# Kernel optimization log

Hardware: AMD Instinct MI355X
Metric: run time of the kernel (lower is better)

The kernel has to match this reference:

```python
import jax, jax.numpy as jnp
import numpy as np
import math

N_HEADS = 8

def setup_inputs() -> dict:
    key = jax.random.key(0)
    ks = jax.random.split(key, 5)
    B, S, D = 2, 2048, 512
    return {
        "x": jax.random.normal(ks[0], (B, S, D), dtype=jnp.float32),
        "w_in": jax.random.normal(ks[1], (3 * D, D), dtype=jnp.float32) * (1.0 / math.sqrt(D)),
        "b_in": jax.random.normal(ks[2], (3 * D,), dtype=jnp.float32) * 0.01,
        "w_out": jax.random.normal(ks[3], (D, D), dtype=jnp.float32) * (1.0 / math.sqrt(D)),
        "b_out": jax.random.normal(ks[4], (D,), dtype=jnp.float32) * 0.01,
        "casual_mask": 1,
    }

def reference(x, w_in, b_in, w_out, b_out, casual_mask):
    B, S, D = x.shape
    H = N_HEADS
    dh = D // H
    # in_proj: torch Linear -> x @ W.T + b
    qvk = x @ w_in.T + b_in  # [B, S, 3D]
    # NOTE: source unpacks as q, v, k (chunk order quirk preserved)
    q, v, k = jnp.split(qvk, 3, axis=-1)
    # [B, S, D] -> [B, H, S, dh]
    def to_heads(t):
        return t.reshape(B, S, H, dh).transpose(0, 2, 1, 3)
    q, k, v = to_heads(q), to_heads(k), to_heads(v)
    scores = jnp.einsum("bhqd,bhkd->bhqk", q, k)  # [B, H, S, S]
    if casual_mask:
        # mask BEFORE scaling, as in the source (-inf unaffected by division)
        tri = jnp.triu(jnp.ones((S, S), dtype=bool), k=1)
        scores = jnp.where(tri, -jnp.inf, scores)
    scores = scores / math.sqrt(dh)
    attn = jax.nn.softmax(scores, axis=-1)
    out = jnp.einsum("bhqk,bhkd->bhqd", attn, v)  # [B, H, S, dh]
    out = out.transpose(0, 2, 1, 3).reshape(B, S, D)
    return out @ w_out.T + b_out
```

## Files before the change

### kernel.cpp

```cpp
#include <hip/hip_runtime.h>
#include <hip/hip_bf16.h>

typedef unsigned short u16;
typedef unsigned int u32;
typedef __attribute__((ext_vector_type(8))) short bf16x8;
typedef __attribute__((ext_vector_type(4))) short bf16x4;
typedef __attribute__((ext_vector_type(4))) float f32x4;

#define DEVI __device__ __forceinline__

DEVI u16 f2bf(float f) {
  union { float f; unsigned int u; } v; v.f = f;
  unsigned int u = v.u;
  unsigned int r = (u + 0x7fffu + ((u >> 16) & 1u)) >> 16;
  return (u16)r;
}

DEVI float fexp2(float x) {
#if __has_builtin(__builtin_amdgcn_exp2f)
  return __builtin_amdgcn_exp2f(x);
#else
  return exp2f(x);
#endif
}

DEVI void lds_cp16(u16* lds, const u16* g) {
  __builtin_amdgcn_global_load_lds(
      (const __attribute__((address_space(1))) u32*)g,
      (__attribute__((address_space(3))) u32*)lds, 16, 0, 0);
}

DEVI f32x4 mfma16x16x16_bf16(bf16x4 a, bf16x4 b, f32x4 c) {
#if __has_builtin(__builtin_amdgcn_mfma_f32_16x16x16bf16_1k)
  return __builtin_amdgcn_mfma_f32_16x16x16bf16_1k(a, b, c, 0, 0, 0);
#else
  f32x4 d;
  asm volatile("v_mfma_f32_16x16x16_bf16 %0, %1, %2, %3"
               : "=v"(d) : "v"(a), "v"(b), "v"(c));
  return d;
#endif
}

__global__ __launch_bounds__(256) void cvt_all(
    const float4* __restrict__ x, const float4* __restrict__ wi,
    const float4* __restrict__ wo, u16* __restrict__ xb,
    u16* __restrict__ wib, u16* __restrict__ wob) {
  int i = blockIdx.x * 256 + threadIdx.x;
  const float4* src; u16* dst; int off;
  if (i < 524288)      { src = x;  dst = xb;  off = i; }
  else if (i < 720896) { src = wi; dst = wib; off = i - 524288; }
  else                 { src = wo; dst = wob; off = i - 720896; }
  float4 f = src[off];
  ushort4 o;
  o.x = f2bf(f.x); o.y = f2bf(f.y); o.z = f2bf(f.z); o.w = f2bf(f.w);
  ((ushort4*)dst)[off] = o;
}

__global__ __launch_bounds__(256) void inproj_gemm(
    const u16* __restrict__ xb, const u16* __restrict__ wb,
    const float* __restrict__ bin,
    u16* __restrict__ Qb, u16* __restrict__ Kb, u16* __restrict__ Vrow) {
  const int K = 512;
  __shared__ u16 At[2][128 * 32];
  __shared__ u16 Bt[2][128 * 32];
  int tid = threadIdx.x;
  int w = tid >> 6, lane = tid & 63;
  int ql = lane & 15, quad = lane >> 4;
  int wr = w >> 1, wc = w & 1;
  int mtile = blockIdx.x * 128, ntile = blockIdx.y * 128;

  int r4 = lane >> 2, c4 = lane & 3;
  int swz4 = c4 ^ (r4 & 3);

  const u16* ag0 = xb + (size_t)(mtile + w * 32 + r4) * K + swz4 * 8;
  const u16* bg0 = wb + (size_t)(ntile + w * 32 + r4) * K + swz4 * 8;

  f32x4 acc[4][4];
#pragma unroll
  for (int t = 0; t < 4; ++t)
#pragma unroll
    for (int u = 0; u < 4; ++u) acc[t][u] = (f32x4){0, 0, 0, 0};

  lds_cp16(&At[0][w * 1024], ag0);
  lds_cp16(&At[0][w * 1024 + 512], ag0 + 16 * K);
  lds_cp16(&Bt[0][w * 1024], bg0);
  lds_cp16(&Bt[0][w * 1024 + 512], bg0 + 16 * K);

  int cb = ql & 3;
  for (int kk = 0; kk < 16; ++kk) {
    int cur = kk & 1;
    __syncthreads();
    if (kk < 15) {
      int k0 = (kk + 1) * 32;
      lds_cp16(&At[cur ^ 1][w * 1024], ag0 + k0);
      lds_cp16(&At[cur ^ 1][w * 1024 + 512], ag0 + 16 * K + k0);
      lds_cp16(&Bt[cur ^ 1][w * 1024], bg0 + k0);
      lds_cp16(&Bt[cur ^ 1][w * 1024 + 512], bg0 + 16 * K + k0);
    }
    bf16x8 af[4], bf[4];
#pragma unroll
    for (int t = 0; t < 4; ++t) {
      int row = wr * 64 + t * 16 + ql;
      af[t] = *(const bf16x8*)(&At[cur][row * 32 + ((quad ^ cb) * 8)]);
    }
#pragma unroll
    for (int u = 0; u < 4; ++u) {
      int row = wc * 64 + u * 16 + ql;
      bf[u] = *(const bf16x8*)(&Bt[cur][row * 32 + ((quad ^ cb) * 8)]);
    }
#pragma unroll
    for (int t = 0; t < 4; ++t)
#pragma unroll
      for (int u = 0; u < 4; ++u)
        acc[t][u] = __builtin_amdgcn_mfma_f32_16x16x32_bf16(af[t], bf[u], acc[t][u], 0, 0, 0);
  }

#pragma unroll
  for (int u = 0; u < 4; ++u) {
    int n = ntile + wc * 64 + u * 16 + ql;
    float bias = bin[n];
    int chunk = n >> 9;
    int nc = n & 511;
    int h = nc >> 6, d = nc & 63;
#pragma unroll
    for (int t = 0; t < 4; ++t)
#pragma unroll
      for (int r = 0; r < 4; ++r) {
        int m = mtile + wr * 64 + t * 16 + quad * 4 + r;
        int b = m >> 11, s = m & 2047;
        u16 val = f2bf(acc[t][u][r] + bias);
        size_t idx = (((size_t)(b * 8 + h)) * 2048 + s) * 64 + d;
        if (chunk == 0)      Qb[idx] = val;
        else if (chunk == 2) Kb[idx] = val;
        else                 Vrow[idx] = val;
      }
  }
}

__global__ __launch_bounds__(256) void transpose_v(
    const u16* __restrict__ Vrow, u16* __restrict__ Vt) {
  __shared__ u16 T[64][68];
  int tid = threadIdx.x;
  int stile = blockIdx.x, bh = blockIdx.y;
  const u16* src = Vrow + ((size_t)bh * 2048 + stile * 64) * 64;
  int r = tid >> 3, c = (tid & 7) * 8;
  *(bf16x8*)&T[r][c]      = *(const bf16x8*)(src + r * 64 + c);
  *(bf16x8*)&T[r + 32][c] = *(const bf16x8*)(src + (r + 32) * 64 + c);
  __syncthreads();
  u16* dst = Vt + (size_t)bh * 64 * 2048 + stile * 64;
#pragma unroll
  for (int p = 0; p < 2; ++p) {
    int oc = p * 256 + tid;
    int d = oc >> 3, sc = (oc & 7) * 8;
    union { bf16x8 v; u16 e[8]; } out;
#pragma unroll
    for (int i = 0; i < 8; ++i) out.e[i] = T[sc + i][d];
    *(bf16x8*)(dst + (size_t)d * 2048 + sc) = out.v;
  }
}

__global__ __launch_bounds__(512) void attn_kernel(
    const u16* __restrict__ Qb, const u16* __restrict__ Kb,
    const u16* __restrict__ Vt, u16* __restrict__ Ob) {
  const int S = 2048;
  __shared__ u16 Kt[2][2][4096];
  __shared__ u16 Vl[2][2][4096];
  int tid = threadIdx.x;
  int grp = tid >> 8;
  int w = (tid >> 6) & 3;
  int lane = tid & 63;
  int ql = lane & 15, quad = lane >> 4;
  int tile = 31 - blockIdx.x;
  int bh = blockIdx.y;
  int qbase = tile * 64 + w * 16;
  int q = qbase + ql;
  const u16* Qh = Qb + (size_t)bh * S * 64;
  const u16* Kh = Kb + (size_t)bh * S * 64;
  const u16* Vh = Vt + (size_t)bh * 64 * S;

  int r8 = lane >> 3, c8 = lane & 7;
  int swz = c8 ^ r8;
  int cb = ql & 7;
  const float SCL = 0.180336878f;

  bf16x8 q0 = *(const bf16x8*)(Qh + (size_t)q * 64 + quad * 8);
  bf16x8 q1 = *(const bf16x8*)(Qh + (size_t)q * 64 + 32 + quad * 8);

  f32x4 o[4] = {{0,0,0,0},{0,0,0,0},{0,0,0,0},{0,0,0,0}};
  float m = -3.0e38f, l = 0.0f;
  int half = (tile + 2) >> 1;

  {
    int kb0 = grp * half;
    if (kb0 <= tile) {
      int kbase = kb0 * 64;
      const u16* kg = Kh + (size_t)(kbase + w * 16 + r8) * 64 + swz * 8;
      lds_cp16(&Kt[grp][0][w * 1024], kg);
      lds_cp16(&Kt[grp][0][w * 1024 + 512], kg + 8 * 64);
      const u16* vg = Vh + (size_t)(w * 16 + r8) * S + kbase + swz * 8;
      lds_cp16(&Vl[grp][0][w * 1024], vg);
      lds_cp16(&Vl[grp][0][w * 1024 + 512], vg + 8 * S);
    }
  }

  for (int j = 0; j < half; ++j) {
    int cur = j & 1;
    int kb = grp * half + j;
    bool real = (kb <= tile);
    int kbase = kb * 64;
    __syncthreads();
    {
      int kbn = kb + 1;
      if (j + 1 < half && kbn <= tile) {
        int kn = kbn * 64;
        const u16* kg = Kh + (size_t)(kn + w * 16 + r8) * 64 + swz * 8;
        lds_cp16(&Kt[grp][cur ^ 1][w * 1024], kg);
        lds_cp16(&Kt[grp][cur ^ 1][w * 1024 + 512], kg + 8 * 64);
        const u16* vg = Vh + (size_t)(w * 16 + r8) * S + kn + swz * 8;
        lds_cp16(&Vl[grp][cur ^ 1][w * 1024], vg);
        lds_cp16(&Vl[grp][cur ^ 1][w * 1024 + 512], vg + 8 * S);
      }
    }
    if (!real) continue;
    f32x4 st[4];
#pragma unroll
    for (int t = 0; t < 4; ++t) {
      const u16* kr = &Kt[grp][cur][(t * 16 + ql) * 64];
      bf16x8 kf0 = *(const bf16x8*)(kr + ((quad ^ cb) * 8));
      bf16x8 kf1 = *(const bf16x8*)(kr + (((quad + 4) ^ cb) * 8));
      f32x4 s = {0, 0, 0, 0};
      s = __builtin_amdgcn_mfma_f32_16x16x32_bf16(kf0, q0, s, 0, 0, 0);
      s = __builtin_amdgcn_mfma_f32_16x16x32_bf16(kf1, q1, s, 0, 0, 0);
      st[t] = s;
    }
    bool needmask = (kbase + 63 > qbase);
    float sc[4][4];
#pragma unroll
    for (int t = 0; t < 4; ++t)
#pragma unroll
      for (int r = 0; r < 4; ++r) {
        float v = st[t][r] * SCL;
        if (needmask) {
          int key = kbase + t * 16 + quad * 4 + r;
          if (key > q) v = -3.0e38f;
        }
        sc[t][r] = v;
      }
    float mx = sc[0][0];
#pragma unroll
    for (int t = 0; t < 4; ++t)
#pragma unroll
      for (int r = 0; r < 4; ++r) mx = fmaxf(mx, sc[t][r]);
    mx = fmaxf(mx, __shfl_xor(mx, 16));
    mx = fmaxf(mx, __shfl_xor(mx, 32));
    float mn = fmaxf(m, mx);
    float alpha = fexp2(m - mn);
    m = mn;
    float rs = 0.0f;
    bf16x4 p[4];
#pragma unroll
    for (int t = 0; t < 4; ++t)
#pragma unroll
      for (int r = 0; r < 4; ++r) {
        float e = fexp2(sc[t][r] - mn);
        rs += e;
        p[t][r] = (short)f2bf(e);
      }
    rs += __shfl_xor(rs, 16);
    rs += __shfl_xor(rs, 32);
    l = l * alpha + rs;
#pragma unroll
    for (int d = 0; d < 4; ++d) o[d] *= alpha;
#pragma unroll
    for (int t = 0; t < 4; ++t)
#pragma unroll
      for (int d = 0; d < 4; ++d) {
        const u16* vr = &Vl[grp][cur][(d * 16 + ql) * 64];
        bf16x4 vf = *(const bf16x4*)(vr + (((t * 2 + (quad >> 1)) ^ cb) * 8 + (quad & 1) * 4));
        o[d] = mfma16x16x16_bf16(vf, p[t], o[d]);
      }
  }

  float* ob  = (float*)&Kt[0][0][0];
  float* mlb = (float*)&Vl[0][0][0];
  int lg = tid & 255;
  __syncthreads();
  if (grp == 1) {
#pragma unroll
    for (int d = 0; d < 4; ++d)
#pragma unroll
      for (int r = 0; r < 4; ++r) ob[lg * 16 + d * 4 + r] = o[d][r];
    mlb[lg * 2] = m;
    mlb[lg * 2 + 1] = l;
  }
  __syncthreads();
  if (grp == 0) {
    float mB = mlb[lg * 2], lB = mlb[lg * 2 + 1];
    float M = fmaxf(m, mB);
    float aA = fexp2(m - M), aB = fexp2(mB - M);
    float L = l * aA + lB * aB;
    float inv = 1.0f / L;
    int b = bh >> 3, h = bh & 7;
    size_t row = ((size_t)b * 2048 + q) * 512 + h * 64;
#pragma unroll
    for (int d = 0; d < 4; ++d) {
      ushort4 v;
      v.x = f2bf((o[d][0] * aA + ob[lg * 16 + d * 4 + 0] * aB) * inv);
      v.y = f2bf((o[d][1] * aA + ob[lg * 16 + d * 4 + 1] * aB) * inv);
      v.z = f2bf((o[d][2] * aA + ob[lg * 16 + d * 4 + 2] * aB) * inv);
      v.w = f2bf((o[d][3] * aA + ob[lg * 16 + d * 4 + 3] * aB) * inv);
      *(ushort4*)(Ob + row + d * 16 + quad * 4) = v;
    }
  }
}

__global__ __launch_bounds__(256) void outproj_gemm(
    const u16* __restrict__ Ob, const u16* __restrict__ wb,
    const float* __restrict__ bout, float* __restrict__ out) {
  const int K = 512;
  __shared__ u16 At[2][64 * 32];
  __shared__ u16 Bt[2][128 * 32];
  int tid = threadIdx.x;
  int w = tid >> 6, lane = tid & 63;
  int ql = lane & 15, quad = lane >> 4;
  int wr = w >> 1, wc = w & 1;
  int mtile = blockIdx.x * 64, ntile = blockIdx.y * 128;

  int r4 = lane >> 2, c4 = lane & 3;
  int swz4 = c4 ^ (r4 & 3);

  const u16* ag0 = Ob + (size_t)(mtile + w * 16 + r4) * K + swz4 * 8;
  const u16* bg0 = wb + (size_t)(ntile + w * 32 + r4) * K + swz4 * 8;

  f32x4 acc[2][4];
#pragma unroll
  for (int t = 0; t < 2; ++t)
#pragma unroll
    for (int u = 0; u < 4; ++u) acc[t][u] = (f32x4){0, 0, 0, 0};

  lds_cp16(&At[0][w * 512], ag0);
  lds_cp16(&Bt[0][w * 1024], bg0);
  lds_cp16(&Bt[0][w * 1024 + 512], bg0 + 16 * K);

  int cb = ql & 3;
  for (int kk = 0; kk < 16; ++kk) {
    int cur = kk & 1;
    __syncthreads();
    if (kk < 15) {
      int k0 = (kk + 1) * 32;
      lds_cp16(&At[cur ^ 1][w * 512], ag0 + k0);
      lds_cp16(&Bt[cur ^ 1][w * 1024], bg0 + k0);
      lds_cp16(&Bt[cur ^ 1][w * 1024 + 512], bg0 + 16 * K + k0);
    }
    bf16x8 af[2], bf[4];
#pragma unroll
    for (int t = 0; t < 2; ++t) {
      int row = wr * 32 + t * 16 + ql;
      af[t] = *(const bf16x8*)(&At[cur][row * 32 + ((quad ^ cb) * 8)]);
    }
#pragma unroll
    for (int u = 0; u < 4; ++u) {
      int row = wc * 64 + u * 16 + ql;
      bf[u] = *(const bf16x8*)(&Bt[cur][row * 32 + ((quad ^ cb) * 8)]);
    }
#pragma unroll
    for (int t = 0; t < 2; ++t)
#pragma unroll
      for (int u = 0; u < 4; ++u)
        acc[t][u] = __builtin_amdgcn_mfma_f32_16x16x32_bf16(af[t], bf[u], acc[t][u], 0, 0, 0);
  }

#pragma unroll
  for (int u = 0; u < 4; ++u) {
    int n = ntile + wc * 64 + u * 16 + ql;
    float bias = bout[n];
#pragma unroll
    for (int t = 0; t < 2; ++t)
#pragma unroll
      for (int r = 0; r < 4; ++r) {
        int mm = mtile + wr * 32 + t * 16 + quad * 4 + r;
        out[(size_t)mm * 512 + n] = acc[t][u][r] + bias;
      }
  }
}

extern "C" void kernel_launch(void* const* d_in, const int* in_sizes, int n_in,
                              void* d_out, int out_size, void* d_ws, size_t ws_size,
                              hipStream_t stream) {
  const float* x     = (const float*)d_in[0];
  const float* w_in  = (const float*)d_in[1];
  const float* b_in  = (const float*)d_in[2];
  const float* w_out = (const float*)d_in[3];
  const float* b_out = (const float*)d_in[4];
  float* out = (float*)d_out;
  char* ws = (char*)d_ws;

  u16* xb    = (u16*)(ws);
  u16* winb  = (u16*)(ws + 4194304);
  u16* woutb = (u16*)(ws + 5767168);
  u16* Qb    = (u16*)(ws + 6291456);
  u16* Kb    = (u16*)(ws + 10485760);
  u16* Vt    = (u16*)(ws + 14680064);
  u16* Ob    = (u16*)(ws + 18874368);
  u16* Vrow  = Ob;

  cvt_all<<<3072, 256, 0, stream>>>((const float4*)x, (const float4*)w_in,
                                    (const float4*)w_out, xb, winb, woutb);
  inproj_gemm<<<dim3(32, 12), 256, 0, stream>>>(xb, winb, b_in, Qb, Kb, Vrow);
  transpose_v<<<dim3(32, 16), 256, 0, stream>>>(Vrow, Vt);
  attn_kernel<<<dim3(32, 16), 512, 0, stream>>>(Qb, Kb, Vt, Ob);
  outproj_gemm<<<dim3(64, 4), 256, 0, stream>>>(Ob, woutb, b_out, out);
}
```

Before: 141.7 us.

## Pair causal query tiles per attention block and halve inproj M tile

The attention kernel now gives each block two query tiles, j and 31-j, so every block processes the same total number of 33 key blocks. The two 256-thread groups split that combined work list evenly, and only tile B's partial softmax state has to be merged. The grid shrinks to 16x16 blocks, which removes the causal load imbalance of the old scheme where each block handled one tile split in half. Separately, the in-projection GEMM tile is reduced to 64x128 with twice as many blocks to raise occupancy and parallelism, at the cost of less reuse of the B operand per block.

```diff
diff --git a/kernel.cpp b/kernel.cpp
--- a/kernel.cpp
+++ b/kernel.cpp
@@ -61,28 +61,27 @@
     const float* __restrict__ bin,
     u16* __restrict__ Qb, u16* __restrict__ Kb, u16* __restrict__ Vrow) {
   const int K = 512;
-  __shared__ u16 At[2][128 * 32];
+  __shared__ u16 At[2][64 * 32];
   __shared__ u16 Bt[2][128 * 32];
   int tid = threadIdx.x;
   int w = tid >> 6, lane = tid & 63;
   int ql = lane & 15, quad = lane >> 4;
   int wr = w >> 1, wc = w & 1;
-  int mtile = blockIdx.x * 128, ntile = blockIdx.y * 128;
+  int mtile = blockIdx.x * 64, ntile = blockIdx.y * 128;
 
   int r4 = lane >> 2, c4 = lane & 3;
   int swz4 = c4 ^ (r4 & 3);
 
-  const u16* ag0 = xb + (size_t)(mtile + w * 32 + r4) * K + swz4 * 8;
+  const u16* ag0 = xb + (size_t)(mtile + w * 16 + r4) * K + swz4 * 8;
   const u16* bg0 = wb + (size_t)(ntile + w * 32 + r4) * K + swz4 * 8;
 
-  f32x4 acc[4][4];
-#pragma unroll
-  for (int t = 0; t < 4; ++t)
+  f32x4 acc[2][4];
+#pragma unroll
+  for (int t = 0; t < 2; ++t)
 #pragma unroll
     for (int u = 0; u < 4; ++u) acc[t][u] = (f32x4){0, 0, 0, 0};
 
-  lds_cp16(&At[0][w * 1024], ag0);
-  lds_cp16(&At[0][w * 1024 + 512], ag0 + 16 * K);
+  lds_cp16(&At[0][w * 512], ag0);
   lds_cp16(&Bt[0][w * 1024], bg0);
   lds_cp16(&Bt[0][w * 1024 + 512], bg0 + 16 * K);
 
@@ -92,15 +91,14 @@
     __syncthreads();
     if (kk < 15) {
       int k0 = (kk + 1) * 32;
-      lds_cp16(&At[cur ^ 1][w * 1024], ag0 + k0);
-      lds_cp16(&At[cur ^ 1][w * 1024 + 512], ag0 + 16 * K + k0);
+      lds_cp16(&At[cur ^ 1][w * 512], ag0 + k0);
       lds_cp16(&Bt[cur ^ 1][w * 1024], bg0 + k0);
       lds_cp16(&Bt[cur ^ 1][w * 1024 + 512], bg0 + 16 * K + k0);
     }
-    bf16x8 af[4], bf[4];
-#pragma unroll
-    for (int t = 0; t < 4; ++t) {
-      int row = wr * 64 + t * 16 + ql;
+    bf16x8 af[2], bf[4];
+#pragma unroll
+    for (int t = 0; t < 2; ++t) {
+      int row = wr * 32 + t * 16 + ql;
       af[t] = *(const bf16x8*)(&At[cur][row * 32 + ((quad ^ cb) * 8)]);
     }
 #pragma unroll
@@ -109,7 +107,7 @@
       bf[u] = *(const bf16x8*)(&Bt[cur][row * 32 + ((quad ^ cb) * 8)]);
     }
 #pragma unroll
-    for (int t = 0; t < 4; ++t)
+    for (int t = 0; t < 2; ++t)
 #pragma unroll
       for (int u = 0; u < 4; ++u)
         acc[t][u] = __builtin_amdgcn_mfma_f32_16x16x32_bf16(af[t], bf[u], acc[t][u], 0, 0, 0);
@@ -123,10 +121,10 @@
     int nc = n & 511;
     int h = nc >> 6, d = nc & 63;
 #pragma unroll
-    for (int t = 0; t < 4; ++t)
+    for (int t = 0; t < 2; ++t)
 #pragma unroll
       for (int r = 0; r < 4; ++r) {
-        int m = mtile + wr * 64 + t * 16 + quad * 4 + r;
+        int m = mtile + wr * 32 + t * 16 + quad * 4 + r;
         int b = m >> 11, s = m & 2047;
         u16 val = f2bf(acc[t][u][r] + bias);
         size_t idx = (((size_t)(b * 8 + h)) * 2048 + s) * 64 + d;
@@ -170,10 +168,11 @@
   int w = (tid >> 6) & 3;
   int lane = tid & 63;
   int ql = lane & 15, quad = lane >> 4;
-  int tile = 31 - blockIdx.x;
+  int j = blockIdx.x;
+  int tileA = j, tileB = 31 - j;
   int bh = blockIdx.y;
-  int qbase = tile * 64 + w * 16;
-  int q = qbase + ql;
+  int qbaseA = tileA * 64 + w * 16;
+  int qbaseB = tileB * 64 + w * 16;
   const u16* Qh = Qb + (size_t)bh * S * 64;
   const u16* Kh = Kb + (size_t)bh * S * 64;
   const u16* Vh = Vt + (size_t)bh * 64 * S;
@@ -183,45 +182,26 @@
   int cb = ql & 7;
   const float SCL = 0.180336878f;
 
-  bf16x8 q0 = *(const bf16x8*)(Qh + (size_t)q * 64 + quad * 8);
-  bf16x8 q1 = *(const bf16x8*)(Qh + (size_t)q * 64 + 32 + quad * 8);
-
-  f32x4 o[4] = {{0,0,0,0},{0,0,0,0},{0,0,0,0},{0,0,0,0}};
-  float m = -3.0e38f, l = 0.0f;
-  int half = (tile + 2) >> 1;
-
-  {
-    int kb0 = grp * half;
-    if (kb0 <= tile) {
-      int kbase = kb0 * 64;
-      const u16* kg = Kh + (size_t)(kbase + w * 16 + r8) * 64 + swz * 8;
-      lds_cp16(&Kt[grp][0][w * 1024], kg);
-      lds_cp16(&Kt[grp][0][w * 1024 + 512], kg + 8 * 64);
-      const u16* vg = Vh + (size_t)(w * 16 + r8) * S + kbase + swz * 8;
-      lds_cp16(&Vl[grp][0][w * 1024], vg);
-      lds_cp16(&Vl[grp][0][w * 1024 + 512], vg + 8 * S);
-    }
-  }
-
-  for (int j = 0; j < half; ++j) {
-    int cur = j & 1;
-    int kb = grp * half + j;
-    bool real = (kb <= tile);
-    int kbase = kb * 64;
-    __syncthreads();
-    {
-      int kbn = kb + 1;
-      if (j + 1 < half && kbn <= tile) {
-        int kn = kbn * 64;
-        const u16* kg = Kh + (size_t)(kn + w * 16 + r8) * 64 + swz * 8;
-        lds_cp16(&Kt[grp][cur ^ 1][w * 1024], kg);
-        lds_cp16(&Kt[grp][cur ^ 1][w * 1024 + 512], kg + 8 * 64);
-        const u16* vg = Vh + (size_t)(w * 16 + r8) * S + kn + swz * 8;
-        lds_cp16(&Vl[grp][cur ^ 1][w * 1024], vg);
-        lds_cp16(&Vl[grp][cur ^ 1][w * 1024 + 512], vg + 8 * S);
-      }
-    }
-    if (!real) continue;
+  bf16x8 qA0 = *(const bf16x8*)(Qh + (size_t)(qbaseA + ql) * 64 + quad * 8);
+  bf16x8 qA1 = *(const bf16x8*)(Qh + (size_t)(qbaseA + ql) * 64 + 32 + quad * 8);
+  bf16x8 qB0 = *(const bf16x8*)(Qh + (size_t)(qbaseB + ql) * 64 + quad * 8);
+  bf16x8 qB1 = *(const bf16x8*)(Qh + (size_t)(qbaseB + ql) * 64 + 32 + quad * 8);
+
+  f32x4 oA[4] = {{0,0,0,0},{0,0,0,0},{0,0,0,0},{0,0,0,0}};
+  f32x4 oB[4] = {{0,0,0,0},{0,0,0,0},{0,0,0,0},{0,0,0,0}};
+  float mA = -3.0e38f, lA = 0.0f, mB = -3.0e38f, lB = 0.0f;
+
+  auto stage = [&](int buf, int kbase) {
+    const u16* kg = Kh + (size_t)(kbase + w * 16 + r8) * 64 + swz * 8;
+    lds_cp16(&Kt[grp][buf][w * 1024], kg);
+    lds_cp16(&Kt[grp][buf][w * 1024 + 512], kg + 8 * 64);
+    const u16* vg = Vh + (size_t)(w * 16 + r8) * S + kbase + swz * 8;
+    lds_cp16(&Vl[grp][buf][w * 1024], vg);
+    lds_cp16(&Vl[grp][buf][w * 1024 + 512], vg + 8 * S);
+  };
+  auto process = [&](int cur, int kbase, int qbase, bf16x8 x0, bf16x8 x1,
+                     f32x4 (&o)[4], float& m, float& l) {
+    int q = qbase + ql;
     f32x4 st[4];
 #pragma unroll
     for (int t = 0; t < 4; ++t) {
@@ -229,8 +209,8 @@
       bf16x8 kf0 = *(const bf16x8*)(kr + ((quad ^ cb) * 8));
       bf16x8 kf1 = *(const bf16x8*)(kr + (((quad + 4) ^ cb) * 8));
       f32x4 s = {0, 0, 0, 0};
-      s = __builtin_amdgcn_mfma_f32_16x16x32_bf16(kf0, q0, s, 0, 0, 0);
-      s = __builtin_amdgcn_mfma_f32_16x16x32_bf16(kf1, q1, s, 0, 0, 0);
+      s = __builtin_amdgcn_mfma_f32_16x16x32_bf16(kf0, x0, s, 0, 0, 0);
+      s = __builtin_amdgcn_mfma_f32_16x16x32_bf16(kf1, x1, s, 0, 0, 0);
       st[t] = s;
     }
     bool needmask = (kbase + 63 > qbase);
@@ -279,37 +259,69 @@
         bf16x4 vf = *(const bf16x4*)(vr + (((t * 2 + (quad >> 1)) ^ cb) * 8 + (quad & 1) * 4));
         o[d] = mfma16x16x16_bf16(vf, p[t], o[d]);
       }
+  };
+
+  {
+    int i0 = grp * 17;
+    int kb = (i0 <= tileA) ? i0 : (i0 - tileA - 1);
+    stage(0, kb * 64);
+  }
+
+  for (int r = 0; r < 17; ++r) {
+    int i = grp * 17 + r;
+    int cur = r & 1;
+    __syncthreads();
+    int inext = i + 1;
+    if (r + 1 < 17 && inext < 33) {
+      int kb = (inext <= tileA) ? inext : (inext - tileA - 1);
+      stage(cur ^ 1, kb * 64);
+    }
+    if (i < 33) {
+      if (i <= tileA) process(cur, i * 64, qbaseA, qA0, qA1, oA, mA, lA);
+      else            process(cur, (i - tileA - 1) * 64, qbaseB, qB0, qB1, oB, mB, lB);
+    }
   }
 
   float* ob  = (float*)&Kt[0][0][0];
   float* mlb = (float*)&Vl[0][0][0];
   int lg = tid & 255;
+  int b = bh >> 3, h = bh & 7;
   __syncthreads();
   if (grp == 1) {
 #pragma unroll
     for (int d = 0; d < 4; ++d)
 #pragma unroll
-      for (int r = 0; r < 4; ++r) ob[lg * 16 + d * 4 + r] = o[d][r];
-    mlb[lg * 2] = m;
-    mlb[lg * 2 + 1] = l;
+      for (int r = 0; r < 4; ++r) ob[lg * 16 + d * 4 + r] = oB[d][r];
+    mlb[lg * 2] = mB;
+    mlb[lg * 2 + 1] = lB;
   }
   __syncthreads();
   if (grp == 0) {
-    float mB = mlb[lg * 2], lB = mlb[lg * 2 + 1];
-    float M = fmaxf(m, mB);
-    float aA = fexp2(m - M), aB = fexp2(mB - M);
-    float L = l * aA + lB * aB;
-    float inv = 1.0f / L;
-    int b = bh >> 3, h = bh & 7;
-    size_t row = ((size_t)b * 2048 + q) * 512 + h * 64;
+    float invA = 1.0f / lA;
+    size_t rowA = ((size_t)b * 2048 + qbaseA + ql) * 512 + h * 64;
 #pragma unroll
     for (int d = 0; d < 4; ++d) {
       ushort4 v;
-      v.x = f2bf((o[d][0] * aA + ob[lg * 16 + d * 4 + 0] * aB) * inv);
-      v.y = f2bf((o[d][1] * aA + ob[lg * 16 + d * 4 + 1] * aB) * inv);
-      v.z = f2bf((o[d][2] * aA + ob[lg * 16 + d * 4 + 2] * aB) * inv);
-      v.w = f2bf((o[d][3] * aA + ob[lg * 16 + d * 4 + 3] * aB) * inv);
-      *(ushort4*)(Ob + row + d * 16 + quad * 4) = v;
+      v.x = f2bf(oA[d][0] * invA);
+      v.y = f2bf(oA[d][1] * invA);
+      v.z = f2bf(oA[d][2] * invA);
+      v.w = f2bf(oA[d][3] * invA);
+      *(ushort4*)(Ob + rowA + d * 16 + quad * 4) = v;
+    }
+    float mBo = mlb[lg * 2], lBo = mlb[lg * 2 + 1];
+    float M = fmaxf(mB, mBo);
+    float a0 = fexp2(mB - M), a1 = fexp2(mBo - M);
+    float L = lB * a0 + lBo * a1;
+    float inv = 1.0f / L;
+    size_t rowB = ((size_t)b * 2048 + qbaseB + ql) * 512 + h * 64;
+#pragma unroll
+    for (int d = 0; d < 4; ++d) {
+      ushort4 v;
+      v.x = f2bf((oB[d][0] * a0 + ob[lg * 16 + d * 4 + 0] * a1) * inv);
+      v.y = f2bf((oB[d][1] * a0 + ob[lg * 16 + d * 4 + 1] * a1) * inv);
+      v.z = f2bf((oB[d][2] * a0 + ob[lg * 16 + d * 4 + 2] * a1) * inv);
+      v.w = f2bf((oB[d][3] * a0 + ob[lg * 16 + d * 4 + 3] * a1) * inv);
+      *(ushort4*)(Ob + rowB + d * 16 + quad * 4) = v;
     }
   }
 }
@@ -406,8 +418,8 @@
 
   cvt_all<<<3072, 256, 0, stream>>>((const float4*)x, (const float4*)w_in,
                                     (const float4*)w_out, xb, winb, woutb);
-  inproj_gemm<<<dim3(32, 12), 256, 0, stream>>>(xb, winb, b_in, Qb, Kb, Vrow);
+  inproj_gemm<<<dim3(64, 12), 256, 0, stream>>>(xb, winb, b_in, Qb, Kb, Vrow);
   transpose_v<<<dim3(32, 16), 256, 0, stream>>>(Vrow, Vt);
-  attn_kernel<<<dim3(32, 16), 512, 0, stream>>>(Qb, Kb, Vt, Ob);
+  attn_kernel<<<dim3(16, 16), 512, 0, stream>>>(Qb, Kb, Vt, Ob);
   outproj_gemm<<<dim3(64, 4), 256, 0, stream>>>(Ob, woutb, b_out, out);
 }
```

New measurement: 135.5 us. 1.05x faster.
